# Kernel optimization log

Hardware: AMD Instinct MI355X
Metric: run time of the kernel (lower is better)

Reference implementation:

```python
import jax, jax.numpy as jnp
import numpy as np

HID, NH = 2048, 16
QLR, KVLR = 1536, 512
DR, DN, DQK, DV = 64, 128, 192, 128
S = 2048
EPS = 1e-06


def rmsnorm(x, w, eps=EPS):
    return x * jax.lax.rsqrt(jnp.mean(x * x, axis=-1, keepdims=True) + eps) * w


def rope_interleave(x, cos, sin):
    # x: [B,H,S,D]; cos/sin: [B,S,D] (unsqueezed to head dim 1)
    b, h, s, d = x.shape
    # DeepSeek-V3 interleave: (d//2, 2) -> transpose -> flatten
    x = x.reshape(b, h, s, d // 2, 2).swapaxes(3, 4).reshape(b, h, s, d)
    c = cos[:, None, :, :]
    sn = sin[:, None, :, :]
    x1, x2 = x[..., : d // 2], x[..., d // 2:]
    rot = jnp.concatenate([-x2, x1], axis=-1)
    return x * c + rot * sn


def setup_inputs() -> dict:
    key = jax.random.key(0)
    ks = jax.random.split(key, 8)
    hidden_states = jax.random.normal(ks[0], (1, S, HID), dtype=jnp.float32)
    # real RoPE tables for the 64-dim rope part
    inv_freq = 1.0 / (10000.0 ** (np.arange(0, DR, 2, dtype=np.float32) / DR))
    pos = np.arange(S, dtype=np.float32)
    freqs = pos[:, None] * inv_freq[None, :]          # [S, DR/2]
    emb = np.concatenate([freqs, freqs], axis=-1)     # [S, DR]
    cos = jnp.asarray(np.cos(emb), dtype=jnp.float32)[None]
    sin = jnp.asarray(np.sin(emb), dtype=jnp.float32)[None]
    w = 0.02
    wq_a = jax.random.normal(ks[1], (QLR, HID), dtype=jnp.float32) * w
    q_a_ln_w = jnp.ones((QLR,), dtype=jnp.float32)
    wq_b = jax.random.normal(ks[2], (NH * DQK, QLR), dtype=jnp.float32) * w
    wkv_a = jax.random.normal(ks[3], (KVLR + DR, HID), dtype=jnp.float32) * w
    kv_a_ln_w = jnp.ones((KVLR,), dtype=jnp.float32)
    wkv_b = jax.random.normal(ks[4], (NH * (DN + DV), KVLR), dtype=jnp.float32) * w
    wo = jax.random.normal(ks[5], (HID, NH * DV), dtype=jnp.float32) * w
    cu_seqlens = jnp.array([0, S // 2, S], dtype=jnp.int32)  # two packed docs
    return {"hidden_states": hidden_states, "cos": cos, "sin": sin,
            "wq_a": wq_a, "q_a_ln_w": q_a_ln_w, "wq_b": wq_b,
            "wkv_a": wkv_a, "kv_a_ln_w": kv_a_ln_w, "wkv_b": wkv_b,
            "wo": wo, "cu_seqlens": cu_seqlens, "max_seqlen": S // 2}


def reference(hidden_states, cos, sin, wq_a, q_a_ln_w, wq_b, wkv_a, kv_a_ln_w,
              wkv_b, wo, cu_seqlens, max_seqlen):
    B, s, _ = hidden_states.shape
    # LoRA-compressed Q: q_a -> RMSNorm -> q_b
    q = rmsnorm(hidden_states @ wq_a.T, q_a_ln_w) @ wq_b.T       # [B,S,NH*DQK]
    q = q.reshape(B, s, NH, DQK).transpose(0, 2, 1, 3)           # [B,NH,S,DQK]
    q_pass, q_rot = q[..., :DN], q[..., DN:]
    # compressed KV with MQA rope part
    ckv = hidden_states @ wkv_a.T                                 # [B,S,KVLR+DR]
    kv_c, k_rot = ckv[..., :KVLR], ckv[..., KVLR:]
    kv = rmsnorm(kv_c, kv_a_ln_w) @ wkv_b.T                       # [B,S,NH*(DN+DV)]
    kv = kv.reshape(B, s, NH, DN + DV).transpose(0, 2, 1, 3)      # [B,NH,S,DN+DV]
    k_pass, v = kv[..., :DN], kv[..., DN:]
    k_rot = k_rot[:, None, :, :]                                  # [B,1,S,DR]
    q_rot = rope_interleave(q_rot, cos, sin)
    k_rot = rope_interleave(k_rot, cos, sin)
    k_rot = jnp.broadcast_to(k_rot, (B, NH, s, DR))
    qf = jnp.concatenate([q_pass, q_rot], axis=-1)                # [B,NH,S,DQK]
    kf = jnp.concatenate([k_pass, k_rot], axis=-1)                # [B,NH,S,DQK]
    # varlen causal attention: block-diagonal per document + causal
    pos = jnp.arange(s)
    seg = jnp.searchsorted(cu_seqlens[1:], pos, side='right')
    mask = (seg[:, None] == seg[None, :]) & (pos[:, None] >= pos[None, :])
    scale = DQK ** -0.5  # flash default: 1/sqrt(q head dim) (v padded to DQK)
    scores = jnp.einsum('bhqd,bhkd->bhqk', qf, kf) * scale
    scores = jnp.where(mask[None, None], scores, jnp.finfo(scores.dtype).min)
    attn = jax.nn.softmax(scores, axis=-1)
    out = jnp.einsum('bhqk,bhkd->bhqd', attn, v)                  # [B,NH,S,DV]
    out = out.transpose(0, 2, 1, 3).reshape(B, s, NH * DV)
    return out @ wo.T
```

## Files before the change

### kernel.cpp

```cpp
#include <hip/hip_runtime.h>

typedef unsigned short u16;
typedef __attribute__((ext_vector_type(8))) short bf16x8;
typedef __attribute__((ext_vector_type(4))) float f32x4;

#define HID 2048
#define NH 16
#define QLR 1536
#define KVLR 512
#define DR 64
#define DN 128
#define DQK 192
#define DV 128
#define SEQ 2048
#define NKVA 2176
#define SCALE 0.07216878364870323f

static __device__ __forceinline__ u16 f2bf(float f) {
  unsigned v = __builtin_bit_cast(unsigned, f);
  v = v + 0x7fffu + ((v >> 16) & 1u);
  return (u16)(v >> 16);
}
static __device__ __forceinline__ float bf2f(u16 u) {
  unsigned v = ((unsigned)u) << 16;
  return __builtin_bit_cast(float, v);
}

#define GLOAD16(gp, lp)                                                        \
  __builtin_amdgcn_global_load_lds(                                            \
      (const __attribute__((address_space(1))) void*)(gp),                     \
      (__attribute__((address_space(3))) void*)(lp), 16, 0, 0)

__global__ void k_convert(const float* __restrict__ src, u16* __restrict__ dst,
                          long nsrc, long ndst) {
  long i = ((long)blockIdx.x * blockDim.x + threadIdx.x) * 4;
  long stride = (long)gridDim.x * blockDim.x * 4;
  for (; i < ndst; i += stride) {
    u16 o0 = 0, o1 = 0, o2 = 0, o3 = 0;
    if (i < nsrc) {
      const float4 f = *(const float4*)(src + i);
      o0 = f2bf(f.x); o1 = f2bf(f.y); o2 = f2bf(f.z); o3 = f2bf(f.w);
    }
    u16* d = dst + i;
    d[0] = o0; d[1] = o1; d[2] = o2; d[3] = o3;
  }
}

__global__ void k_rmsnorm(const float* __restrict__ X, const float* __restrict__ w,
                          u16* __restrict__ Y, int xstride, int cols, float inv_cols) {
  const int row = blockIdx.x;
  const int t = threadIdx.x;
  const float* x = X + (size_t)row * xstride;
  float ss = 0.f;
  for (int i = t * 4; i < cols; i += 1024) {
    float4 v = *(const float4*)(x + i);
    ss += v.x * v.x + v.y * v.y + v.z * v.z + v.w * v.w;
  }
#pragma unroll
  for (int m = 1; m < 64; m <<= 1) ss += __shfl_xor(ss, m, 64);
  __shared__ float red[4];
  if ((t & 63) == 0) red[t >> 6] = ss;
  __syncthreads();
  float tot = red[0] + red[1] + red[2] + red[3];
  float r = rsqrtf(tot * inv_cols + 1e-6f);
  for (int i = t * 4; i < cols; i += 1024) {
    float4 v = *(const float4*)(x + i);
    float4 g = *(const float4*)(w + i);
    u16* y = Y + (size_t)row * cols + i;
    y[0] = f2bf(v.x * r * g.x);
    y[1] = f2bf(v.y * r * g.y);
    y[2] = f2bf(v.z * r * g.z);
    y[3] = f2bf(v.w * r * g.w);
  }
}

__global__ __launch_bounds__(256) void k_gemm_nt(
    const u16* __restrict__ A, const u16* __restrict__ B, void* __restrict__ Cout,
    int M, int N, int K, int c_bf16) {
  __shared__ __align__(16) u16 As[2][8192];
  __shared__ __align__(16) u16 Bs[2][8192];
  const int t = threadIdx.x;
  const int lane = t & 63;
  const int w = t >> 6, wr = w >> 1, wc = w & 1;
  const int lm = lane & 15, lg = lane >> 4;

  const int nwg = gridDim.x * gridDim.y;
  int bid = blockIdx.y * gridDim.x + blockIdx.x;
  if ((nwg & 7) == 0) bid = (bid & 7) * (nwg >> 3) + (bid >> 3);
  const int bm = bid % gridDim.y;
  const int bn = bid / gridDim.y;

  const int srow = t >> 3;
  const int scol = ((t & 7) ^ (srow & 7)) * 8;
  const u16* aBase = A + (size_t)(bm * 128 + srow) * K + scol;
  const u16* bBase = B + (size_t)(bn * 128 + srow) * K + scol;
  const size_t rowStep = (size_t)32 * K;

#define STAGE(buf, kt_)                                                        \
  do {                                                                         \
    _Pragma("unroll") for (int p = 0; p < 4; ++p) {                            \
      GLOAD16(aBase + (kt_) + p * rowStep, (u16*)As[buf] + p * 2048 + t * 8);  \
      GLOAD16(bBase + (kt_) + p * rowStep, (u16*)Bs[buf] + p * 2048 + t * 8);  \
    }                                                                          \
  } while (0)

  f32x4 acc[4][4] = {};
  const int nk = K >> 6;
  STAGE(0, 0);
  if (nk > 1) STAGE(1, 64);
  int cur = 0;
  for (int kt = 0; kt < nk; ++kt) {
    if (kt + 1 < nk) asm volatile("s_waitcnt vmcnt(8)" ::: "memory");
    else             asm volatile("s_waitcnt vmcnt(0)" ::: "memory");
    __builtin_amdgcn_s_barrier();
    __builtin_amdgcn_sched_barrier(0);
    bf16x8 af[2][4], bfr[2][4];
#pragma unroll
    for (int kk = 0; kk < 2; ++kk) {
#pragma unroll
      for (int i = 0; i < 4; ++i) {
        const int row_ = wr * 64 + i * 16 + lm;
        af[kk][i] = *(const bf16x8*)(As[cur] + row_ * 64 +
                                     ((((kk << 2) | lg) ^ (row_ & 7)) << 3));
      }
#pragma unroll
      for (int j = 0; j < 4; ++j) {
        const int row_ = wc * 64 + j * 16 + lm;
        bfr[kk][j] = *(const bf16x8*)(Bs[cur] + row_ * 64 +
                                      ((((kk << 2) | lg) ^ (row_ & 7)) << 3));
      }
    }
    asm volatile("s_waitcnt lgkmcnt(0)" ::: "memory");
    __builtin_amdgcn_sched_barrier(0);
    __builtin_amdgcn_s_barrier();
    __builtin_amdgcn_sched_barrier(0);
    if (kt + 2 < nk) STAGE(cur, (kt + 2) << 6);
    __builtin_amdgcn_s_setprio(1);
#pragma unroll
    for (int kk = 0; kk < 2; ++kk)
#pragma unroll
      for (int i = 0; i < 4; ++i)
#pragma unroll
        for (int j = 0; j < 4; ++j)
          acc[i][j] = __builtin_amdgcn_mfma_f32_16x16x32_bf16(af[kk][i], bfr[kk][j],
                                                              acc[i][j], 0, 0, 0);
    __builtin_amdgcn_s_setprio(0);
    cur ^= 1;
  }
#undef STAGE

  const int row0 = bm * 128 + wr * 64 + lg * 4;
  const int col0 = bn * 128 + wc * 64 + lm;
  if (c_bf16) {
    u16* C = (u16*)Cout;
#pragma unroll
    for (int i = 0; i < 4; ++i)
#pragma unroll
      for (int r = 0; r < 4; ++r) {
        u16* crow = C + (size_t)(row0 + i * 16 + r) * N + col0;
#pragma unroll
        for (int j = 0; j < 4; ++j) crow[j * 16] = f2bf(acc[i][j][r]);
      }
  } else {
    float* C = (float*)Cout;
#pragma unroll
    for (int i = 0; i < 4; ++i)
#pragma unroll
      for (int r = 0; r < 4; ++r) {
        float* crow = C + (size_t)(row0 + i * 16 + r) * N + col0;
#pragma unroll
        for (int j = 0; j < 4; ++j) crow[j * 16] = acc[i][j][r];
      }
  }
}

__global__ void k_mk_qf(const u16* __restrict__ qfull, const float* __restrict__ cosb,
                        const float* __restrict__ sinb, u16* __restrict__ qf) {
  const int s = blockIdx.x, h = blockIdx.y, t = threadIdx.x;
  const u16* src = qfull + (size_t)s * (NH * DQK) + h * DQK;
  u16* dst = qf + ((size_t)h * SEQ + s) * DQK;
  dst[t] = f2bf(bf2f(src[t]) * SCALE);
  if (t < 32) {
    float a = bf2f(src[DN + 2 * t]);
    float b = bf2f(src[DN + 2 * t + 1]);
    float c = cosb[(size_t)s * DR + t];
    float sn = sinb[(size_t)s * DR + t];
    dst[DN + t] = f2bf((a * c - b * sn) * SCALE);
    dst[DN + 32 + t] = f2bf((b * c + a * sn) * SCALE);
  }
}

__global__ void k_mk_kf_v(const u16* __restrict__ kvfull, const float* __restrict__ krot,
                          int krot_stride, const float* __restrict__ cosb,
                          const float* __restrict__ sinb, u16* __restrict__ kf,
                          u16* __restrict__ vt) {
  const int s = blockIdx.x, h = blockIdx.y, t = threadIdx.x;
  const u16* src = kvfull + (size_t)s * (NH * 256) + h * 256;
  u16* kdst = kf + ((size_t)h * SEQ + s) * DQK;
  kdst[t] = src[t];
  vt[((size_t)h * DV + t) * SEQ + s] = src[DN + t];
  if (t < 32) {
    float a = krot[(size_t)s * krot_stride + 2 * t];
    float b = krot[(size_t)s * krot_stride + 2 * t + 1];
    float c = cosb[(size_t)s * DR + t];
    float sn = sinb[(size_t)s * DR + t];
    kdst[DN + t] = f2bf(a * c - b * sn);
    kdst[DN + 32 + t] = f2bf(b * c + a * sn);
  }
}

__global__ __launch_bounds__(256) void k_attn(
    const u16* __restrict__ qf, const u16* __restrict__ kf, const u16* __restrict__ vt,
    u16* __restrict__ attn_out) {
  __shared__ __align__(16) u16 Ks[2][32 * 192];
  __shared__ __align__(16) u16 Vs[2][128 * 32];
  __shared__ __align__(16) u16 p_lds[4][16][32];

  const int t = threadIdx.x, lane = t & 63, w = t >> 6;
  const int lm = lane & 15, lg = lane >> 4;
  const int bid = blockIdx.x;
  const int x = bid & 7, r0 = bid >> 3;
  const int h = x * 2 + (r0 & 1);
  const int u = r0 >> 1;
  const int seg = u & 1;
  const int tj = 15 - (u >> 1);
  const int tile_row0 = seg * 1024 + tj * 64;
  const int k_begin = seg * 1024;
  const int n_kt = tj * 2 + 2;

  const int lo_row = tile_row0 + w * 16;
  bf16x8 qfr[6];
  {
    const u16* qp = qf + ((size_t)h * SEQ + (lo_row + lm)) * DQK + lg * 8;
#pragma unroll
    for (int c = 0; c < 6; ++c) qfr[c] = *(const bf16x8*)(qp + c * 32);
  }
  int qrow[4];
#pragma unroll
  for (int r = 0; r < 4; ++r) qrow[r] = lo_row + lg * 4 + r;

  float m_r[4], l_loc[4];
#pragma unroll
  for (int r = 0; r < 4; ++r) { m_r[r] = -3.0e4f; l_loc[r] = 0.f; }
  f32x4 oacc[8] = {};

#define STAGE(buf, kt_)                                                        \
  do {                                                                         \
    const int k0_ = k_begin + (kt_) * 32;                                      \
    _Pragma("unroll") for (int p = 0; p < 3; ++p) {                            \
      const int id = p * 256 + t;                                              \
      const int row = id / 24, colL = id - row * 24;                           \
      const u16* g = kf + ((size_t)h * SEQ + k0_ + row) * DQK +                \
                     ((colL ^ (row & 7)) * 8);                                 \
      GLOAD16(g, (u16*)Ks[buf] + id * 8);                                      \
    }                                                                          \
    _Pragma("unroll") for (int p = 0; p < 2; ++p) {                            \
      const int id = p * 256 + t;                                              \
      const int row = id >> 2, colL = id & 3;                                  \
      const u16* g = vt + ((size_t)h * DV + row) * SEQ + k0_ +                 \
                     ((colL ^ (row & 3)) * 8);                                 \
      GLOAD16(g, (u16*)Vs[buf] + id * 8);                                      \
    }                                                                          \
  } while (0)

#define COMPUTE(buf, kt_)                                                      \
  do {                                                                         \
    const int k0_ = k_begin + (kt_) * 32;                                      \
    f32x4 sc[2] = {};                                                          \
    __builtin_amdgcn_s_setprio(1);                                             \
    _Pragma("unroll") for (int n0_ = 0; n0_ < 2; ++n0_)                        \
        _Pragma("unroll") for (int c_ = 0; c_ < 6; ++c_) {                     \
      const int row_ = n0_ * 16 + lm, cc_ = c_ * 4 + lg;                       \
      bf16x8 kfr = *(const bf16x8*)(Ks[buf] + row_ * 192 +                     \
                                    ((cc_ ^ (row_ & 7)) * 8));                 \
      sc[n0_] = __builtin_amdgcn_mfma_f32_16x16x32_bf16(qfr[c_], kfr,          \
                                                        sc[n0_], 0, 0, 0);     \
    }                                                                          \
    __builtin_amdgcn_s_setprio(0);                                             \
    float s0a[4], s1a[4];                                                      \
    float over = -1e30f;                                                       \
    if (lo_row >= k0_ + 31) {     \
      _Pragma("unroll") for (int r = 0; r < 4; ++r) {                          \
        s0a[r] = sc[0][r];                                                     \
        s1a[r] = sc[1][r];                                                     \
        over = fmaxf(over, fmaxf(s0a[r], s1a[r]) - m_r[r]);                    \
      }                                                                        \
    } else {                                                                   \
      const int kc0 = k0_ + lm, kc1 = k0_ + 16 + lm;                           \
      _Pragma("unroll") for (int r = 0; r < 4; ++r) {                          \
        s0a[r] = (kc0 <= qrow[r]) ? sc[0][r] : -1e30f;                         \
        s1a[r] = (kc1 <= qrow[r]) ? sc[1][r] : -1e30f;                         \
        over = fmaxf(over, fmaxf(s0a[r], s1a[r]) - m_r[r]);                    \
      }                                                                        \
    }                                                                          \
    if (__any(over > 8.0f)) {                                                  \
      _Pragma("unroll") for (int r = 0; r < 4; ++r) {                          \
        float mx = fmaxf(s0a[r], s1a[r]);                                      \
        _Pragma("unroll") for (int md = 1; md < 16; md <<= 1)                  \
            mx = fmaxf(mx, __shfl_xor(mx, md, 64));                            \
        float mnew = fmaxf(m_r[r], mx);                                        \
        float alpha = __expf(m_r[r] - mnew);                                   \
        m_r[r] = mnew;                                                         \
        l_loc[r] *= alpha;                                                     \
        _Pragma("unroll") for (int nd = 0; nd < 8; ++nd) oacc[nd][r] *= alpha; \
      }                                                                        \
    }                                                                          \
    _Pragma("unroll") for (int r = 0; r < 4; ++r) {                            \
      float p0 = __expf(s0a[r] - m_r[r]);                                      \
      float p1 = __expf(s1a[r] - m_r[r]);                                      \
      l_loc[r] += p0 + p1;                                                     \
      p_lds[w][lg * 4 + r][lm] = f2bf(p0);                                     \
      p_lds[w][lg * 4 + r][16 + lm] = f2bf(p1);                                \
    }                                                                          \
    asm volatile("s_waitcnt lgkmcnt(0)" ::: "memory");                         \
    __builtin_amdgcn_sched_barrier(0);                                         \
    bf16x8 pa = *(const bf16x8*)(&p_lds[w][lm][lg * 8]);                       \
    __builtin_amdgcn_s_setprio(1);                                             \
    _Pragma("unroll") for (int nd = 0; nd < 8; ++nd) {                         \
      const int row_ = nd * 16 + lm;                                           \
      bf16x8 vvf = *(const bf16x8*)(Vs[buf] + row_ * 32 +                      \
                                    ((lg ^ (row_ & 3)) * 8));                  \
      oacc[nd] =                                                               \
          __builtin_amdgcn_mfma_f32_16x16x32_bf16(pa, vvf, oacc[nd], 0, 0, 0); \
    }                                                                          \
    __builtin_amdgcn_s_setprio(0);                                             \
  } while (0)

  int cur = 0;
  STAGE(0, 0);
  STAGE(1, 1);
  for (int kt = 0; kt < n_kt; ++kt) {
    if (kt + 1 < n_kt) asm volatile("s_waitcnt vmcnt(5)" ::: "memory");
    else               asm volatile("s_waitcnt vmcnt(0)" ::: "memory");
    __builtin_amdgcn_s_barrier();
    __builtin_amdgcn_sched_barrier(0);
    COMPUTE(cur, kt);
    asm volatile("s_waitcnt lgkmcnt(0)" ::: "memory");
    __builtin_amdgcn_sched_barrier(0);
    __builtin_amdgcn_s_barrier();
    __builtin_amdgcn_sched_barrier(0);
    if (kt + 2 < n_kt) STAGE(cur, kt + 2);
    cur ^= 1;
  }
#undef STAGE
#undef COMPUTE

#pragma unroll
  for (int r = 0; r < 4; ++r) {
    float lt = l_loc[r];
#pragma unroll
    for (int md = 1; md < 16; md <<= 1) lt += __shfl_xor(lt, md, 64);
    float inv = 1.0f / lt;
#pragma unroll
    for (int nd = 0; nd < 8; ++nd)
      attn_out[(size_t)qrow[r] * (NH * DV) + h * DV + nd * 16 + lm] =
          f2bf(oacc[nd][r] * inv);
  }
}

extern "C" void kernel_launch(void* const* d_in, const int* in_sizes, int n_in,
                              void* d_out, int out_size, void* d_ws, size_t ws_size,
                              hipStream_t stream) {
  const float* hs = (const float*)d_in[0];
  const float* cosb = (const float*)d_in[1];
  const float* sinb = (const float*)d_in[2];
  const float* wq_a = (const float*)d_in[3];
  const float* q_a_ln_w = (const float*)d_in[4];
  const float* wq_b = (const float*)d_in[5];
  const float* wkv_a = (const float*)d_in[6];
  const float* kv_a_ln_w = (const float*)d_in[7];
  const float* wkv_b = (const float*)d_in[8];
  const float* wo = (const float*)d_in[9];

  char* ws = (char*)d_ws;
  size_t off = 0;
  auto take = [&](size_t bytes) {
    size_t o = off;
    off += (bytes + 255) & ~(size_t)255;
    return o;
  };
  u16* hs_bf = (u16*)(ws + take((size_t)SEQ * HID * 2));
  u16* wqkva = (u16*)(ws + take((size_t)NKVA * HID * 2));
  u16* wqb = (u16*)(ws + take((size_t)(NH * DQK) * QLR * 2));
  u16* wkvb = (u16*)(ws + take((size_t)(NH * 256) * KVLR * 2));
  u16* wo_bf = (u16*)(ws + take((size_t)HID * (NH * DV) * 2));
  float* qkva = (float*)(ws + take((size_t)SEQ * NKVA * 4));
  u16* q_ln = (u16*)(ws + take((size_t)SEQ * QLR * 2));
  u16* kv_ln = (u16*)(ws + take((size_t)SEQ * KVLR * 2));
  u16* qfull = (u16*)(ws + take((size_t)SEQ * NH * DQK * 2));
  u16* kvfull = (u16*)(ws + take((size_t)SEQ * NH * 256 * 2));
  u16* qf = (u16*)(ws + take((size_t)NH * SEQ * DQK * 2));
  u16* kf = (u16*)(ws + take((size_t)NH * SEQ * DQK * 2));
  u16* vt = (u16*)(ws + take((size_t)NH * DV * SEQ * 2));
  u16* attn = (u16*)(ws + take((size_t)SEQ * NH * DV * 2));
  if (off > ws_size) return;

  auto blocks4 = [](long n) {
    long b = (n / 4 + 255) / 256;
    return (int)(b > 4096 ? 4096 : b);
  };

  k_convert<<<blocks4((long)SEQ * HID), 256, 0, stream>>>(hs, hs_bf, (long)SEQ * HID, (long)SEQ * HID);
  k_convert<<<blocks4((long)QLR * HID), 256, 0, stream>>>(wq_a, wqkva, (long)QLR * HID, (long)QLR * HID);
  k_convert<<<blocks4((long)640 * HID), 256, 0, stream>>>(wkv_a, wqkva + (size_t)QLR * HID,
                                                          (long)(KVLR + DR) * HID, (long)640 * HID);
  k_convert<<<blocks4((long)NH * DQK * QLR), 256, 0, stream>>>(wq_b, wqb, (long)NH * DQK * QLR,
                                                               (long)NH * DQK * QLR);
  k_convert<<<blocks4((long)NH * 256 * KVLR), 256, 0, stream>>>(wkv_b, wkvb, (long)NH * 256 * KVLR,
                                                                (long)NH * 256 * KVLR);
  k_convert<<<blocks4((long)HID * NH * DV), 256, 0, stream>>>(wo, wo_bf, (long)HID * NH * DV,
                                                              (long)HID * NH * DV);

  dim3 g1(NKVA / 128, SEQ / 128);
  k_gemm_nt<<<g1, 256, 0, stream>>>(hs_bf, wqkva, qkva, SEQ, NKVA, HID, 0);

  k_rmsnorm<<<SEQ, 256, 0, stream>>>(qkva, q_a_ln_w, q_ln, NKVA, QLR, 1.0f / QLR);
  k_rmsnorm<<<SEQ, 256, 0, stream>>>(qkva + QLR, kv_a_ln_w, kv_ln, NKVA, KVLR, 1.0f / KVLR);

  dim3 g2(NH * DQK / 128, SEQ / 128);
  k_gemm_nt<<<g2, 256, 0, stream>>>(q_ln, wqb, qfull, SEQ, NH * DQK, QLR, 1);
  dim3 g3(NH * 256 / 128, SEQ / 128);
  k_gemm_nt<<<g3, 256, 0, stream>>>(kv_ln, wkvb, kvfull, SEQ, NH * 256, KVLR, 1);

  k_mk_qf<<<dim3(SEQ, NH), 128, 0, stream>>>(qfull, cosb, sinb, qf);
  k_mk_kf_v<<<dim3(SEQ, NH), 128, 0, stream>>>(kvfull, qkva + (QLR + KVLR), NKVA, cosb, sinb, kf, vt);

  k_attn<<<512, 256, 0, stream>>>(qf, kf, vt, attn);

  dim3 g4(HID / 128, SEQ / 128);
  k_gemm_nt<<<g4, 256, 0, stream>>>(attn, wo_bf, d_out, SEQ, HID, NH * DV, 0);
}
```

Baseline: 221.6 us.

## Split-K first GEMM, wider 512-thread GEMM tiles, tiled V transpose, attention reorder

```diff
diff --git a/kernel.cpp b/kernel.cpp
--- a/kernel.cpp
+++ b/kernel.cpp
@@ -76,7 +76,7 @@
 
 __global__ __launch_bounds__(256) void k_gemm_nt(
     const u16* __restrict__ A, const u16* __restrict__ B, void* __restrict__ Cout,
-    int M, int N, int K, int c_bf16) {
+    int M, int N, int K, int klen, int mode) {
   __shared__ __align__(16) u16 As[2][8192];
   __shared__ __align__(16) u16 Bs[2][8192];
   const int t = threadIdx.x;
@@ -89,11 +89,12 @@
   if ((nwg & 7) == 0) bid = (bid & 7) * (nwg >> 3) + (bid >> 3);
   const int bm = bid % gridDim.y;
   const int bn = bid / gridDim.y;
+  const int k0 = blockIdx.z * klen;
 
   const int srow = t >> 3;
   const int scol = ((t & 7) ^ (srow & 7)) * 8;
-  const u16* aBase = A + (size_t)(bm * 128 + srow) * K + scol;
-  const u16* bBase = B + (size_t)(bn * 128 + srow) * K + scol;
+  const u16* aBase = A + (size_t)(bm * 128 + srow) * K + scol + k0;
+  const u16* bBase = B + (size_t)(bn * 128 + srow) * K + scol + k0;
   const size_t rowStep = (size_t)32 * K;
 
 #define STAGE(buf, kt_)                                                        \
@@ -105,7 +106,7 @@
   } while (0)
 
   f32x4 acc[4][4] = {};
-  const int nk = K >> 6;
+  const int nk = klen >> 6;
   STAGE(0, 0);
   if (nk > 1) STAGE(1, 64);
   int cur = 0;
@@ -151,7 +152,7 @@
 
   const int row0 = bm * 128 + wr * 64 + lg * 4;
   const int col0 = bn * 128 + wc * 64 + lm;
-  if (c_bf16) {
+  if (mode == 1) {
     u16* C = (u16*)Cout;
 #pragma unroll
     for (int i = 0; i < 4; ++i)
@@ -161,6 +162,16 @@
 #pragma unroll
         for (int j = 0; j < 4; ++j) crow[j * 16] = f2bf(acc[i][j][r]);
       }
+  } else if (mode == 0) {
+    float* C = (float*)Cout;
+#pragma unroll
+    for (int i = 0; i < 4; ++i)
+#pragma unroll
+      for (int r = 0; r < 4; ++r) {
+        float* crow = C + (size_t)(row0 + i * 16 + r) * N + col0;
+#pragma unroll
+        for (int j = 0; j < 4; ++j) crow[j * 16] = acc[i][j][r];
+      }
   } else {
     float* C = (float*)Cout;
 #pragma unroll
@@ -169,9 +180,103 @@
       for (int r = 0; r < 4; ++r) {
         float* crow = C + (size_t)(row0 + i * 16 + r) * N + col0;
 #pragma unroll
-        for (int j = 0; j < 4; ++j) crow[j * 16] = acc[i][j][r];
-      }
-  }
+        for (int j = 0; j < 4; ++j) unsafeAtomicAdd(&crow[j * 16], acc[i][j][r]);
+      }
+  }
+}
+
+template <int WN>
+__global__ __launch_bounds__(512) void k_gemm_nt8(
+    const u16* __restrict__ A, const u16* __restrict__ B, u16* __restrict__ C,
+    int M, int N, int K) {
+  constexpr int BN = WN * 64;
+  __shared__ __align__(16) u16 As[2][128 * 64];
+  __shared__ __align__(16) u16 Bs[2][BN * 64];
+  const int t = threadIdx.x;
+  const int lane = t & 63;
+  const int w = t >> 6, wr = w >> 2, wc = w & 3;
+  const int lm = lane & 15, lg = lane >> 4;
+
+  const int nwg = gridDim.x * gridDim.y;
+  int bid = blockIdx.y * gridDim.x + blockIdx.x;
+  if ((nwg & 7) == 0) bid = (bid & 7) * (nwg >> 3) + (bid >> 3);
+  const int bm = bid % gridDim.y;
+  const int bn = bid / gridDim.y;
+
+  const u16* aT = A + (size_t)bm * 128 * K;
+  const u16* bT = B + (size_t)bn * BN * K;
+
+#define STAGE8(buf, kt_)                                                       \
+  do {                                                                         \
+    _Pragma("unroll") for (int i = 0; i < 2; ++i) {                            \
+      const int g = t + i * 512, row = g >> 3, slot = (g & 7) ^ (row & 7);     \
+      GLOAD16(aT + (size_t)row * K + slot * 8 + (kt_), (u16*)As[buf] + g * 8); \
+    }                                                                          \
+    _Pragma("unroll") for (int i = 0; i < WN; ++i) {                           \
+      const int g = t + i * 512, row = g >> 3, slot = (g & 7) ^ (row & 7);     \
+      GLOAD16(bT + (size_t)row * K + slot * 8 + (kt_), (u16*)Bs[buf] + g * 8); \
+    }                                                                          \
+  } while (0)
+
+  f32x4 acc[4][WN] = {};
+  const int nk = K >> 6;
+  STAGE8(0, 0);
+  if (nk > 1) STAGE8(1, 64);
+  int cur = 0;
+  for (int kt = 0; kt < nk; ++kt) {
+    if (kt + 1 < nk) {
+      if constexpr (WN == 3) asm volatile("s_waitcnt vmcnt(5)" ::: "memory");
+      else                   asm volatile("s_waitcnt vmcnt(6)" ::: "memory");
+    } else {
+      asm volatile("s_waitcnt vmcnt(0)" ::: "memory");
+    }
+    __builtin_amdgcn_s_barrier();
+    __builtin_amdgcn_sched_barrier(0);
+    bf16x8 af[2][4], bfr[2][WN];
+#pragma unroll
+    for (int kk = 0; kk < 2; ++kk) {
+#pragma unroll
+      for (int i = 0; i < 4; ++i) {
+        const int row_ = wr * 64 + i * 16 + lm;
+        af[kk][i] = *(const bf16x8*)(As[cur] + row_ * 64 +
+                                     ((((kk << 2) | lg) ^ (row_ & 7)) << 3));
+      }
+#pragma unroll
+      for (int j = 0; j < WN; ++j) {
+        const int row_ = wc * (WN * 16) + j * 16 + lm;
+        bfr[kk][j] = *(const bf16x8*)(Bs[cur] + row_ * 64 +
+                                      ((((kk << 2) | lg) ^ (row_ & 7)) << 3));
+      }
+    }
+    asm volatile("s_waitcnt lgkmcnt(0)" ::: "memory");
+    __builtin_amdgcn_sched_barrier(0);
+    __builtin_amdgcn_s_barrier();
+    __builtin_amdgcn_sched_barrier(0);
+    if (kt + 2 < nk) STAGE8(cur, (kt + 2) << 6);
+    __builtin_amdgcn_s_setprio(1);
+#pragma unroll
+    for (int kk = 0; kk < 2; ++kk)
+#pragma unroll
+      for (int i = 0; i < 4; ++i)
+#pragma unroll
+        for (int j = 0; j < WN; ++j)
+          acc[i][j] = __builtin_amdgcn_mfma_f32_16x16x32_bf16(af[kk][i], bfr[kk][j],
+                                                              acc[i][j], 0, 0, 0);
+    __builtin_amdgcn_s_setprio(0);
+    cur ^= 1;
+  }
+#undef STAGE8
+
+  const int row0 = bm * 128 + wr * 64 + lg * 4;
+  const int col0 = bn * BN + wc * (WN * 16) + lm;
+#pragma unroll
+  for (int i = 0; i < 4; ++i)
+#pragma unroll
+    for (int r = 0; r < 4; ++r) {
+      u16* crow = C + (size_t)(row0 + i * 16 + r) * N + col0;
+#pragma unroll
+      for (int j = 0; j < WN; ++j) crow[j * 16] = f2bf(acc[i][j][r]);
+    }
 }
 
 __global__ void k_mk_qf(const u16* __restrict__ qfull, const float* __restrict__ cosb,
@@ -190,22 +295,44 @@
   }
 }
 
-__global__ void k_mk_kf_v(const u16* __restrict__ kvfull, const float* __restrict__ krot,
-                          int krot_stride, const float* __restrict__ cosb,
-                          const float* __restrict__ sinb, u16* __restrict__ kf,
-                          u16* __restrict__ vt) {
-  const int s = blockIdx.x, h = blockIdx.y, t = threadIdx.x;
-  const u16* src = kvfull + (size_t)s * (NH * 256) + h * 256;
-  u16* kdst = kf + ((size_t)h * SEQ + s) * DQK;
-  kdst[t] = src[t];
-  vt[((size_t)h * DV + t) * SEQ + s] = src[DN + t];
-  if (t < 32) {
-    float a = krot[(size_t)s * krot_stride + 2 * t];
-    float b = krot[(size_t)s * krot_stride + 2 * t + 1];
-    float c = cosb[(size_t)s * DR + t];
-    float sn = sinb[(size_t)s * DR + t];
-    kdst[DN + t] = f2bf(a * c - b * sn);
-    kdst[DN + 32 + t] = f2bf(b * c + a * sn);
+__global__ __launch_bounds__(256) void k_mk_kf_v(
+    const u16* __restrict__ kvfull, const float* __restrict__ krot, int krot_stride,
+    const float* __restrict__ cosb, const float* __restrict__ sinb,
+    u16* __restrict__ kf, u16* __restrict__ vt) {
+  __shared__ u16 vts[128][66];
+  const int s0 = blockIdx.x * 64, h = blockIdx.y, t = threadIdx.x;
+#pragma unroll
+  for (int i = 0; i < 8; ++i) {
+    const int g = t + i * 256, row = g >> 5, slot = g & 31;
+    const u16* src = kvfull + (size_t)(s0 + row) * (NH * 256) + h * 256 + slot * 8;
+    bf16x8 v = *(const bf16x8*)src;
+    if (slot < 16) {
+      *(bf16x8*)(kf + ((size_t)h * SEQ + s0 + row) * DQK + slot * 8) = v;
+    } else {
+      const int d = (slot - 16) * 8;
+#pragma unroll
+      for (int e = 0; e < 8; ++e) vts[d + e][row] = (u16)v[e];
+    }
+  }
+#pragma unroll
+  for (int i = 0; i < 8; ++i) {
+    const int g = t + i * 256, row = g >> 5, c = g & 31;
+    float a = krot[(size_t)(s0 + row) * krot_stride + 2 * c];
+    float b = krot[(size_t)(s0 + row) * krot_stride + 2 * c + 1];
+    float cc = cosb[(size_t)(s0 + row) * DR + c];
+    float sn = sinb[(size_t)(s0 + row) * DR + c];
+    u16* kd = kf + ((size_t)h * SEQ + s0 + row) * DQK;
+    kd[DN + c] = f2bf(a * cc - b * sn);
+    kd[DN + 32 + c] = f2bf(b * cc + a * sn);
+  }
+  __syncthreads();
+#pragma unroll
+  for (int i = 0; i < 4; ++i) {
+    const int g = t + i * 256, d = g >> 3, slot = g & 7;
+    bf16x8 v;
+#pragma unroll
+    for (int e = 0; e < 8; ++e) v[e] = (short)vts[d][slot * 8 + e];
+    *(bf16x8*)(vt + ((size_t)h * DV + d) * SEQ + s0 + slot * 8) = v;
   }
 }
 
@@ -219,11 +346,11 @@
   const int t = threadIdx.x, lane = t & 63, w = t >> 6;
   const int lm = lane & 15, lg = lane >> 4;
   const int bid = blockIdx.x;
-  const int x = bid & 7, r0 = bid >> 3;
-  const int h = x * 2 + (r0 & 1);
-  const int u = r0 >> 1;
-  const int seg = u & 1;
-  const int tj = 15 - (u >> 1);
+  const int x = bid & 7, rr = bid >> 3;
+  const int i5 = rr & 31, late = rr >> 5;
+  const int tj = late ? (i5 >> 2) : 15 - (i5 >> 2);
+  const int h = x * 2 + ((i5 >> 1) & 1);
+  const int seg = i5 & 1;
   const int tile_row0 = seg * 1024 + tj * 64;
   const int k_begin = seg * 1024;
   const int n_kt = tj * 2 + 2;
@@ -279,7 +406,7 @@
     __builtin_amdgcn_s_setprio(0);                                             \
     float s0a[4], s1a[4];                                                      \
     float over = -1e30f;                                                       \
-    if (lo_row >= k0_ + 31) {     \
+    if (lo_row >= k0_ + 31) {                                                  \
       _Pragma("unroll") for (int r = 0; r < 4; ++r) {                          \
         s0a[r] = sc[0][r];                                                     \
         s1a[r] = sc[1][r];                                                     \
@@ -411,22 +538,24 @@
   k_convert<<<blocks4((long)HID * NH * DV), 256, 0, stream>>>(wo, wo_bf, (long)HID * NH * DV,
                                                               (long)HID * NH * DV);
 
-  dim3 g1(NKVA / 128, SEQ / 128);
-  k_gemm_nt<<<g1, 256, 0, stream>>>(hs_bf, wqkva, qkva, SEQ, NKVA, HID, 0);
+  hipMemsetAsync(qkva, 0, (size_t)SEQ * NKVA * 4, stream);
+  dim3 g1(NKVA / 128, SEQ / 128, 2);
+  k_gemm_nt<<<g1, 256, 0, stream>>>(hs_bf, wqkva, qkva, SEQ, NKVA, HID, HID / 2, 2);
 
   k_rmsnorm<<<SEQ, 256, 0, stream>>>(qkva, q_a_ln_w, q_ln, NKVA, QLR, 1.0f / QLR);
   k_rmsnorm<<<SEQ, 256, 0, stream>>>(qkva + QLR, kv_a_ln_w, kv_ln, NKVA, KVLR, 1.0f / KVLR);
 
-  dim3 g2(NH * DQK / 128, SEQ / 128);
-  k_gemm_nt<<<g2, 256, 0, stream>>>(q_ln, wqb, qfull, SEQ, NH * DQK, QLR, 1);
-  dim3 g3(NH * 256 / 128, SEQ / 128);
-  k_gemm_nt<<<g3, 256, 0, stream>>>(kv_ln, wkvb, kvfull, SEQ, NH * 256, KVLR, 1);
+  dim3 g2(NH * DQK / 192, SEQ / 128);
+  k_gemm_nt8<3><<<g2, 512, 0, stream>>>(q_ln, wqb, qfull, SEQ, NH * DQK, QLR);
+  dim3 g3(NH * 256 / 256, SEQ / 128);
+  k_gemm_nt8<4><<<g3, 512, 0, stream>>>(kv_ln, wkvb, kvfull, SEQ, NH * 256, KVLR);
 
   k_mk_qf<<<dim3(SEQ, NH), 128, 0, stream>>>(qfull, cosb, sinb, qf);
-  k_mk_kf_v<<<dim3(SEQ, NH), 128, 0, stream>>>(kvfull, qkva + (QLR + KVLR), NKVA, cosb, sinb, kf, vt);
+  k_mk_kf_v<<<dim3(SEQ / 64, NH), 256, 0, stream>>>(kvfull, qkva + (QLR + KVLR), NKVA,
+                                                    cosb, sinb, kf, vt);
 
   k_attn<<<512, 256, 0, stream>>>(qf, kf, vt, attn);
 
-  dim3 g4(HID / 128, SEQ / 128);
-  k_gemm_nt<<<g4, 256, 0, stream>>>(attn, wo_bf, d_out, SEQ, HID, NH * DV, 0);
-}
+  dim3 g4(HID / 128, SEQ / 128, 1);
+  k_gemm_nt<<<g4, 256, 0, stream>>>(attn, wo_bf, d_out, SEQ, HID, NH * DV, NH * DV, 0);
+}
```

Result: slower. 230.3 us (+3.9%).
